# Optimization experiments

Measured on AMD Instinct MI355X. Metric: run time of the kernel, lower is better.

The kernel has to match this reference:

```python
import jax, jax.numpy as jnp
import numpy as np

H = 32  # hidden_size


def setup_inputs() -> dict:
    key = jax.random.key(0)
    ks = jax.random.split(key, 9)
    B, T = 4096, 512
    s = 1.0 / np.sqrt(H)  # PyTorch-style init scale
    return {
        "x": jax.random.normal(ks[0], (B, T, 1), jnp.float32),
        "W_ih": jax.random.uniform(ks[1], (4 * H, 1), jnp.float32, -s, s),
        "W_hh": jax.random.uniform(ks[2], (4 * H, H), jnp.float32, -s, s),
        "b_ih": jax.random.uniform(ks[3], (4 * H,), jnp.float32, -s, s),
        "b_hh": jax.random.uniform(ks[4], (4 * H,), jnp.float32, -s, s),
        "fc1_w": jax.random.uniform(ks[5], (16, H), jnp.float32, -s, s),
        "fc1_b": jax.random.uniform(ks[6], (16,), jnp.float32, -s, s),
        "fc2_w": jax.random.uniform(ks[7], (1, 16), jnp.float32, -0.25, 0.25),
        "fc2_b": jax.random.uniform(ks[8], (1,), jnp.float32, -0.25, 0.25),
    }


def _lstm_last_h(x, W_ih, W_hh, b_ih, b_hh):
    B, T, _ = x.shape
    # Precompute input projections for all timesteps: [B, T, 4H]
    xg = jnp.einsum('bti,gi->btg', x, W_ih) + b_ih + b_hh
    xg_t = jnp.swapaxes(xg, 0, 1)  # [T, B, 4H] for scan

    def step(carry, xg_step):
        h, c = carry
        gates = xg_step + h @ W_hh.T  # [B, 4H]
        i, f, g, o = jnp.split(gates, 4, axis=-1)  # PyTorch gate order i,f,g,o
        i = jax.nn.sigmoid(i)
        f = jax.nn.sigmoid(f)
        g = jnp.tanh(g)
        o = jax.nn.sigmoid(o)
        c = f * c + i * g
        h = o * jnp.tanh(c)
        return (h, c), None

    h0 = jnp.zeros((B, H), x.dtype)
    c0 = jnp.zeros((B, H), x.dtype)
    (h_last, _), _ = jax.lax.scan(step, (h0, c0), xg_t)
    return h_last  # == output[:, -1, :]


def reference(x, W_ih, W_hh, b_ih, b_hh, fc1_w, fc1_b, fc2_w, fc2_b):
    h = _lstm_last_h(x, W_ih, W_hh, b_ih, b_hh)        # [B, H]
    z = jax.nn.relu(h @ fc1_w.T + fc1_b)               # [B, 16]
    return z @ fc2_w.T + fc2_b                         # [B, 1]
```

## Files before the change

### kernel.cpp

```cpp
#include <hip/hip_runtime.h>

#define TT 512

typedef _Float16 f16x8 __attribute__((ext_vector_type(8)));
typedef float f32x4 __attribute__((ext_vector_type(4)));

__device__ __forceinline__ float fast_exp2(float v) { return __builtin_amdgcn_exp2f(v); }
__device__ __forceinline__ float fast_rcp(float v)  { return __builtin_amdgcn_rcpf(v); }

__global__ __launch_bounds__(64, 1) void lstm_ls4_kernel(
    const float* __restrict__ x,
    const float* __restrict__ wih,
    const float* __restrict__ whh,
    const float* __restrict__ bih,
    const float* __restrict__ bhh,
    const float* __restrict__ fc1w,
    const float* __restrict__ fc1b,
    const float* __restrict__ fc2w,
    const float* __restrict__ fc2b,
    float* __restrict__ out)
{
    __shared__ float lds_xT[TT + 1][4];
    __shared__ float lds_hf[4][32];

    const int lane = threadIdx.x;
    const int b0 = blockIdx.x * 4;
    const int c  = lane & 15;
    const int cb = c & 3;
    const int g  = c >> 2;
    const int q  = lane >> 4;

    {
        const int rb = lane >> 4;
        const int m  = lane & 15;
        const float4* xr = reinterpret_cast<const float4*>(x + (size_t)(b0 + rb) * TT);
#pragma unroll
        for (int it = 0; it < 8; ++it) {
            const int idx = it * 16 + m;
            const float4 v = xr[idx];
            const int t0 = idx * 4;
            lds_xT[t0 + 0][rb] = v.x;
            lds_xT[t0 + 1][rb] = v.y;
            lds_xT[t0 + 2][rb] = v.z;
            lds_xT[t0 + 3][rb] = v.w;
        }
        if (lane < 4) lds_xT[TT][lane] = 0.0f;
    }

    const float NK  = -1.4426950408889634f;
    const float NK2 = -2.8853900817779268f;

    f16x8 afrag[8];
#pragma unroll
    for (int n = 0; n < 8; ++n) {
        const float s = (n == 4 || n == 5) ? NK2 : NK;
        const float* src = whh + (n * 16 + c) * 32;
        f16x8 a;
#pragma unroll
        for (int j = 0; j < 8; ++j)
            a[j] = (_Float16)(s * src[4 * q + (j >> 1) + 16 * (j & 1)]);
        afrag[n] = a;
    }

    float wq[8], bq[8];
#pragma unroll
    for (int n = 0; n < 8; ++n) {
        const float s = (n == 4 || n == 5) ? NK2 : NK;
        const int gg = n * 16 + q * 4 + g;
        wq[n] = s * wih[gg];
        bq[n] = s * (bih[gg] + bhh[gg]);
    }

    const int ba0 = 4 * (cb + 0  + 16 * q);
    const int ba1 = 4 * (cb + 4  + 16 * q);
    const int ba2 = 4 * (cb + 8  + 16 * q);
    const int ba3 = 4 * (cb + 12 + 16 * q);

    f16x8 bfrag;
#pragma unroll
    for (int j = 0; j < 8; ++j) bfrag[j] = (_Float16)0.0f;

    float cst0 = 0.0f, cst1 = 0.0f;
    const f32x4 zero4 = {0.0f, 0.0f, 0.0f, 0.0f};
    const bool gl = (g & 1) != 0;
    const bool gh = (g & 2) != 0;

    float xv = lds_xT[0][cb];

#pragma unroll 1
    for (int t = 0; t < TT; ++t) {
        f32x4 acc[8];
#pragma unroll
        for (int n = 0; n < 8; ++n)
            acc[n] = __builtin_amdgcn_mfma_f32_16x16x32_f16(afrag[n], bfrag, zero4, 0, 0, 0);

        const float xnext = lds_xT[t + 1][cb];

        float v[8];
#pragma unroll
        for (int n = 0; n < 8; ++n) {
            const float lo = gl ? acc[n][1] : acc[n][0];
            const float hi = gl ? acc[n][3] : acc[n][2];
            v[n] = (gh ? hi : lo) + __builtin_fmaf(xv, wq[n], bq[n]);
        }

        float hv0, hv1;
#pragma unroll
        for (int p = 0; p < 2; ++p) {
            const float ei = fast_exp2(v[0 + p]);
            const float ef = fast_exp2(v[2 + p]);
            const float eg = fast_exp2(v[4 + p]);
            const float eo = fast_exp2(v[6 + p]);
            const float P  = (1.0f + ei) * (1.0f + eg);
            const float Bf = 1.0f + ef;
            float& cs = p ? cst1 : cst0;
            const float N  = __builtin_fmaf(cs, P, (1.0f - eg) * Bf);
            const float cn = N * fast_rcp(P * Bf);
            cs = cn;
            const float ec = fast_exp2(NK2 * cn);
            const float hh = (1.0f - ec) * fast_rcp((1.0f + eo) * (1.0f + ec));
            if (p == 0) hv0 = hh; else hv1 = hh;
        }

        const int w = (int)__builtin_bit_cast(unsigned, __builtin_amdgcn_cvt_pkrtz(hv0, hv1));
        uint4 bw;
        bw.x = (unsigned)__builtin_amdgcn_ds_bpermute(ba0, w);
        bw.y = (unsigned)__builtin_amdgcn_ds_bpermute(ba1, w);
        bw.z = (unsigned)__builtin_amdgcn_ds_bpermute(ba2, w);
        bw.w = (unsigned)__builtin_amdgcn_ds_bpermute(ba3, w);
        bfrag = __builtin_bit_cast(f16x8, bw);

        xv = xnext;
    }

    if (c < 4) {
#pragma unroll
        for (int j = 0; j < 8; ++j)
            lds_hf[c][4 * q + (j >> 1) + 16 * (j & 1)] = (float)bfrag[j];
    }

    const int bat = lane >> 4;
    const int m   = lane & 15;
    float s = fc1b[m];
    const float* fw = fc1w + m * 32;
#pragma unroll 8
    for (int u = 0; u < 32; ++u) s = __builtin_fmaf(lds_hf[bat][u], fw[u], s);
    float val = fmaxf(s, 0.0f) * fc2w[m];
    val += __shfl_xor(val, 1);
    val += __shfl_xor(val, 2);
    val += __shfl_xor(val, 4);
    val += __shfl_xor(val, 8);
    if (m == 0) out[b0 + bat] = val + fc2b[0];
}

extern "C" void kernel_launch(void* const* d_in, const int* in_sizes, int n_in,
                              void* d_out, int out_size, void* d_ws, size_t ws_size,
                              hipStream_t stream) {
    const float* x    = (const float*)d_in[0];
    const float* wih  = (const float*)d_in[1];
    const float* whh  = (const float*)d_in[2];
    const float* bih  = (const float*)d_in[3];
    const float* bhh  = (const float*)d_in[4];
    const float* fc1w = (const float*)d_in[5];
    const float* fc1b = (const float*)d_in[6];
    const float* fc2w = (const float*)d_in[7];
    const float* fc2b = (const float*)d_in[8];
    float* out = (float*)d_out;

    const int B = out_size;
    dim3 grid(B / 4), block(64);
    hipLaunchKernelGGL(lstm_ls4_kernel, grid, block, 0, stream,
                       x, wih, whh, bih, bhh, fc1w, fc1b, fc2w, fc2b, out);
}
```

Before: 172.5 us.

## Process two batch rows per wave instead of four, one gate pair per lane

Each 64-lane block now handles 2 batch rows instead of 4, doubling the grid. Each lane evaluates a single hidden unit's nonlinearity instead of two, and a DPP row-rotate swaps values between lane halves to build the packed f16 B fragment. Launch bounds allow two waves per SIMD, so more waves can hide the latency of the serial per-step chain. The cost is that the MFMA work per step stays the same while covering half as many rows, so total matrix-instruction count doubles.

```diff
diff --git a/kernel.cpp b/kernel.cpp
--- a/kernel.cpp
+++ b/kernel.cpp
@@ -8,7 +8,14 @@
 __device__ __forceinline__ float fast_exp2(float v) { return __builtin_amdgcn_exp2f(v); }
 __device__ __forceinline__ float fast_rcp(float v)  { return __builtin_amdgcn_rcpf(v); }
 
-__global__ __launch_bounds__(64, 1) void lstm_ls4_kernel(
+template <int CTRL>
+__device__ __forceinline__ float dppmovf(float v) {
+    return __builtin_bit_cast(float, (unsigned)__builtin_amdgcn_update_dpp(
+        0, (int)__builtin_bit_cast(unsigned, v), CTRL, 0xF, 0xF, true));
+}
+#define DPP_ROR8 0x128
+
+__global__ __launch_bounds__(64, 2) void lstm_ls2_kernel(
     const float* __restrict__ x,
     const float* __restrict__ wih,
     const float* __restrict__ whh,
@@ -20,23 +27,25 @@
     const float* __restrict__ fc2b,
     float* __restrict__ out)
 {
-    __shared__ float lds_xT[TT + 1][4];
-    __shared__ float lds_hf[4][32];
+    __shared__ float lds_xT[TT + 2][2];
+    __shared__ float lds_hf[2][32];
 
     const int lane = threadIdx.x;
-    const int b0 = blockIdx.x * 4;
+    const int b0 = blockIdx.x * 2;
     const int c  = lane & 15;
-    const int cb = c & 3;
-    const int g  = c >> 2;
+    const int cb = c & 1;
+    const int g  = c >> 1;
     const int q  = lane >> 4;
+    const int r  = g & 3;
+    const int p  = g >> 2;
 
     {
-        const int rb = lane >> 4;
-        const int m  = lane & 15;
+        const int rb = lane >> 5;
+        const int m  = lane & 31;
         const float4* xr = reinterpret_cast<const float4*>(x + (size_t)(b0 + rb) * TT);
 #pragma unroll
-        for (int it = 0; it < 8; ++it) {
-            const int idx = it * 16 + m;
+        for (int it = 0; it < 4; ++it) {
+            const int idx = it * 32 + m;
             const float4 v = xr[idx];
             const int t0 = idx * 4;
             lds_xT[t0 + 0][rb] = v.x;
@@ -44,7 +53,7 @@
             lds_xT[t0 + 2][rb] = v.z;
             lds_xT[t0 + 3][rb] = v.w;
         }
-        if (lane < 4) lds_xT[TT][lane] = 0.0f;
+        if (lane < 4) lds_xT[TT + (lane >> 1)][lane & 1] = 0.0f;
     }
 
     const float NK  = -1.4426950408889634f;
@@ -62,28 +71,29 @@
         afrag[n] = a;
     }
 
-    float wq[8], bq[8];
+    float wq[4], bq[4];
 #pragma unroll
-    for (int n = 0; n < 8; ++n) {
-        const float s = (n == 4 || n == 5) ? NK2 : NK;
-        const int gg = n * 16 + q * 4 + g;
-        wq[n] = s * wih[gg];
-        bq[n] = s * (bih[gg] + bhh[gg]);
+    for (int gt = 0; gt < 4; ++gt) {
+        const float s = (gt == 2) ? NK2 : NK;
+        const int gg = (2 * gt + p) * 16 + q * 4 + r;
+        wq[gt] = s * wih[gg];
+        bq[gt] = s * (bih[gg] + bhh[gg]);
     }
 
-    const int ba0 = 4 * (cb + 0  + 16 * q);
-    const int ba1 = 4 * (cb + 4  + 16 * q);
-    const int ba2 = 4 * (cb + 8  + 16 * q);
-    const int ba3 = 4 * (cb + 12 + 16 * q);
+    const int ba0 = 4 * (16 * q + 0 + cb);
+    const int ba1 = 4 * (16 * q + 2 + cb);
+    const int ba2 = 4 * (16 * q + 4 + cb);
+    const int ba3 = 4 * (16 * q + 6 + cb);
 
     f16x8 bfrag;
 #pragma unroll
     for (int j = 0; j < 8; ++j) bfrag[j] = (_Float16)0.0f;
 
-    float cst0 = 0.0f, cst1 = 0.0f;
+    float cs = 0.0f;
     const f32x4 zero4 = {0.0f, 0.0f, 0.0f, 0.0f};
-    const bool gl = (g & 1) != 0;
-    const bool gh = (g & 2) != 0;
+    const bool rl = (r & 1) != 0;
+    const bool rh = (r & 2) != 0;
+    const bool pp = (p != 0);
 
     float xv = lds_xT[0][cb];
 
@@ -96,33 +106,35 @@
 
         const float xnext = lds_xT[t + 1][cb];
 
-        float v[8];
+        float ex[8];
 #pragma unroll
         for (int n = 0; n < 8; ++n) {
-            const float lo = gl ? acc[n][1] : acc[n][0];
-            const float hi = gl ? acc[n][3] : acc[n][2];
-            v[n] = (gh ? hi : lo) + __builtin_fmaf(xv, wq[n], bq[n]);
+            const float lo = rl ? acc[n][1] : acc[n][0];
+            const float hi = rl ? acc[n][3] : acc[n][2];
+            ex[n] = rh ? hi : lo;
         }
+        const float vi = __builtin_fmaf(xv, wq[0], bq[0]) + (pp ? ex[1] : ex[0]);
+        const float vf = __builtin_fmaf(xv, wq[1], bq[1]) + (pp ? ex[3] : ex[2]);
+        const float vg = __builtin_fmaf(xv, wq[2], bq[2]) + (pp ? ex[5] : ex[4]);
+        const float vo = __builtin_fmaf(xv, wq[3], bq[3]) + (pp ? ex[7] : ex[6]);
 
-        float hv0, hv1;
-#pragma unroll
-        for (int p = 0; p < 2; ++p) {
-            const float ei = fast_exp2(v[0 + p]);
-            const float ef = fast_exp2(v[2 + p]);
-            const float eg = fast_exp2(v[4 + p]);
-            const float eo = fast_exp2(v[6 + p]);
-            const float P  = (1.0f + ei) * (1.0f + eg);
-            const float Bf = 1.0f + ef;
-            float& cs = p ? cst1 : cst0;
-            const float N  = __builtin_fmaf(cs, P, (1.0f - eg) * Bf);
-            const float cn = N * fast_rcp(P * Bf);
-            cs = cn;
-            const float ec = fast_exp2(NK2 * cn);
-            const float hh = (1.0f - ec) * fast_rcp((1.0f + eo) * (1.0f + ec));
-            if (p == 0) hv0 = hh; else hv1 = hh;
-        }
+        const float ei = fast_exp2(vi);
+        const float ef = fast_exp2(vf);
+        const float eg = fast_exp2(vg);
+        const float eo = fast_exp2(vo);
+        const float P  = (1.0f + ei) * (1.0f + eg);
+        const float Bf = 1.0f + ef;
+        const float N  = __builtin_fmaf(cs, P, (1.0f - eg) * Bf);
+        const float cn = N * fast_rcp(P * Bf);
+        cs = cn;
+        const float ec = fast_exp2(NK2 * cn);
+        const float hv = (1.0f - ec) * fast_rcp((1.0f + eo) * (1.0f + ec));
 
-        const int w = (int)__builtin_bit_cast(unsigned, __builtin_amdgcn_cvt_pkrtz(hv0, hv1));
+        const float ho = dppmovf<DPP_ROR8>(hv);
+        const float hlo = pp ? ho : hv;
+        const float hhi = pp ? hv : ho;
+        const int w = (int)__builtin_bit_cast(unsigned, __builtin_amdgcn_cvt_pkrtz(hlo, hhi));
+
         uint4 bw;
         bw.x = (unsigned)__builtin_amdgcn_ds_bpermute(ba0, w);
         bw.y = (unsigned)__builtin_amdgcn_ds_bpermute(ba1, w);
@@ -133,19 +145,22 @@
         xv = xnext;
     }
 
-    if (c < 4) {
+    if (c < 2) {
 #pragma unroll
         for (int j = 0; j < 8; ++j)
             lds_hf[c][4 * q + (j >> 1) + 16 * (j & 1)] = (float)bfrag[j];
     }
 
-    const int bat = lane >> 4;
-    const int m   = lane & 15;
-    float s = fc1b[m];
-    const float* fw = fc1w + m * 32;
+    const int bat = lane >> 5;
+    const int m   = lane & 31;
+    float val = 0.0f;
+    if (m < 16) {
+        float s = fc1b[m];
+        const float* fw = fc1w + m * 32;
 #pragma unroll 8
-    for (int u = 0; u < 32; ++u) s = __builtin_fmaf(lds_hf[bat][u], fw[u], s);
-    float val = fmaxf(s, 0.0f) * fc2w[m];
+        for (int u = 0; u < 32; ++u) s = __builtin_fmaf(lds_hf[bat][u], fw[u], s);
+        val = fmaxf(s, 0.0f) * fc2w[m];
+    }
     val += __shfl_xor(val, 1);
     val += __shfl_xor(val, 2);
     val += __shfl_xor(val, 4);
@@ -168,7 +183,7 @@
     float* out = (float*)d_out;
 
     const int B = out_size;
-    dim3 grid(B / 4), block(64);
-    hipLaunchKernelGGL(lstm_ls4_kernel, grid, block, 0, stream,
+    dim3 grid(B / 2), block(64);
+    hipLaunchKernelGGL(lstm_ls2_kernel, grid, block, 0, stream,
                        x, wih, whh, bih, bhh, fc1w, fc1b, fc2w, fc2b, out);
 }
```

New measurement: 194.0 us. +12.5%, slower.
